# Kernel tuning notes

Measured on AMD Instinct MI355X. Metric: run time of the kernel, lower is better.

## Reference

```python
import jax, jax.numpy as jnp
import numpy as np

N, M, A, O, F = 4, 64, 64, 5, 256


def _sph_harm_l2(R):
    # real spherical harmonics up to l=2 (9 components) of the unit direction
    r = jnp.linalg.norm(R, axis=-1, keepdims=True)
    u = R / (r + 1e-12)
    x, y, z = u[..., 0], u[..., 1], u[..., 2]
    c1 = 0.4886025119029199
    c2 = 1.0925484305920792
    return jnp.stack([
        jnp.full_like(x, 0.28209479177387814),
        c1 * y, c1 * z, c1 * x,
        c2 * x * y, c2 * y * z,
        0.31539156525252005 * (3.0 * z * z - 1.0),
        c2 * x * z,
        0.5462742152960396 * (x * x - y * y),
    ], axis=-1)  # [..., 9]


def setup_inputs() -> dict:
    key = jax.random.key(0)
    ks = jax.random.split(key, 6)
    return {
        "ao_embeddings": jax.random.normal(ks[0], (N, M, A, O, F), jnp.float32),
        "C": jax.random.normal(ks[1], (N, M, A, O), jnp.float32),
        "S": jax.random.normal(ks[2], (N, A, 3, A, 3), jnp.float32),
        "R": jax.random.normal(ks[3], (N, M, A, 3), jnp.float32),
        "w_stack": jax.random.normal(ks[4], (5, 3, 3), jnp.float32) * 0.5,
        "cgc": jax.random.normal(ks[5], (9, 9, 9), jnp.float32) * 0.1,
    }


def reference(ao_embeddings, C, S, R, w_stack, cgc):
    # mo_features: [n, m, a, o=5, f]
    mo = C[..., None] * ao_embeddings
    # 5-step bilinear transform of the overlap-like tensor S [n, a, 3, b, 3]
    Sc = S
    for i in range(5):
        w = w_stack[i]  # [3, 3]
        Sc = jnp.einsum('ab,cd,kibjd->kiajc', w, w, Sc)
        Sc = jax.nn.swish(Sc)
    filt = jnp.array([[1., 1., 0.], [1., 1., 0.], [0., 0., 1.]], Sc.dtype)
    Sc = filt[None, None, :, None, :] * Sc
    idx = jnp.array([0, 1, 2, 2, 2])  # tf.repeat(repeats=[1, 1, 3]) -> size 5
    Sc = jnp.take(jnp.take(Sc, idx, axis=2), idx, axis=4)  # [n, a, 5, b, 5]
    # message passing over atom pairs: [n, m, b, p=5, f]
    mo = jnp.einsum('nmaof,naobp->nmbpf', mo, Sc)
    # unsorted_segment_sum with segment_ids [0,0,1,2,3] into 9 slots == matmul with one-hot map
    seg = jnp.zeros((5, 9), mo.dtype).at[jnp.arange(5), jnp.array([0, 0, 1, 2, 3])].set(1.0)
    mo = jnp.einsum('nmbpf,pq->nmbqf', mo, seg)  # [n, m, a, 9, f]
    # coupling: sph harmonics * ||C|| (tf.repeat over f == broadcast, folded into einsum)
    Cn = jnp.linalg.norm(C, axis=-1)            # [n, m, a]
    coup = _sph_harm_l2(R) * Cn[..., None]      # [n, m, a, 9]
    # CG contraction + sum over atoms a: [n, m, i=9, f]
    out = jnp.einsum('nmapf,nmak,kip->nmif', mo, coup, cgc)
    return jnp.transpose(out, (0, 1, 3, 2))     # [n, m, f, 9]
```

## Files before the change

kernel.cpp:

```cpp
#include <hip/hip_runtime.h>
#include <math.h>


typedef float v4f __attribute__((ext_vector_type(4)));
static __device__ inline v4f splat4(float s) { return (v4f){s, s, s, s}; }

__global__ void k_sc(const float* __restrict__ S, const float* __restrict__ wst,
                     float* __restrict__ G) {
    int t = blockIdx.x * 128 + threadIdx.x;
    int n = t >> 12;
    int a = (t >> 6) & 63;
    int b = t & 63;
    float M[3][3];
#pragma unroll
    for (int x = 0; x < 3; ++x)
#pragma unroll
        for (int y = 0; y < 3; ++y)
            M[x][y] = S[(((n * 64 + a) * 3 + x) * 64 + b) * 3 + y];
#pragma unroll
    for (int it = 0; it < 5; ++it) {
        float w[3][3];
#pragma unroll
        for (int x = 0; x < 3; ++x)
#pragma unroll
            for (int y = 0; y < 3; ++y)
                w[x][y] = wst[it * 9 + x * 3 + y];
        float T[3][3];
#pragma unroll
        for (int x = 0; x < 3; ++x)
#pragma unroll
            for (int d = 0; d < 3; ++d)
                T[x][d] = w[x][0] * M[0][d] + w[x][1] * M[1][d] + w[x][2] * M[2][d];
#pragma unroll
        for (int x = 0; x < 3; ++x)
#pragma unroll
            for (int c = 0; c < 3; ++c) {
                float v = T[x][0] * w[c][0] + T[x][1] * w[c][1] + T[x][2] * w[c][2];
                M[x][c] = v / (1.f + expf(-v));
            }
    }
    float g0 = M[0][0] + M[0][1];
    float g1 = M[1][0] + M[1][1];
    float gz = M[2][2];
    size_t base = (size_t)n * 12288 + (size_t)b * 64 + a;
    G[base]          = g0;
    G[base + 4096]   = g1;
    G[base + 8192]   = gz;
}

__global__ __launch_bounds__(576) void k_w3(
        const float* __restrict__ C, const float* __restrict__ R,
        const float* __restrict__ cgc, const float* __restrict__ G,
        float* __restrict__ wsW3) {
    __shared__ float s_coup[64 * 9];
    __shared__ float s_D[2 * 9 * 64];
    __shared__ float s_W3[64 * 27];

    const int nm = blockIdx.x;
    const int n = nm >> 6;
    const int tid = threadIdx.x;

    if (tid < 64) {
        const int b = tid;
        const float* rp = R + ((size_t)nm * 64 + b) * 3;
        float x = rp[0], y = rp[1], z = rp[2];
        float rn = sqrtf(x * x + y * y + z * z) + 1e-12f;
        x /= rn; y /= rn; z /= rn;
        const float* cp = C + ((size_t)nm * 64 + b) * 5;
        float cn = 0.f;
#pragma unroll
        for (int o = 0; o < 5; ++o) cn += cp[o] * cp[o];
        cn = sqrtf(cn);
        const float c1 = 0.4886025119029199f;
        const float c2 = 1.0925484305920792f;
        float Y[9];
        Y[0] = 0.28209479177387814f;
        Y[1] = c1 * y;
        Y[2] = c1 * z;
        Y[3] = c1 * x;
        Y[4] = c2 * x * y;
        Y[5] = c2 * y * z;
        Y[6] = 0.31539156525252005f * (3.f * z * z - 1.f);
        Y[7] = c2 * x * z;
        Y[8] = 0.5462742152960396f * (x * x - y * y);
#pragma unroll
        for (int k = 0; k < 9; ++k) s_coup[b * 9 + k] = Y[k] * cn;
    }
    __syncthreads();

    {
        const int b = tid & 63, i = tid >> 6;
        float d0 = 0.f, dz = 0.f;
#pragma unroll
        for (int k = 0; k < 9; ++k) {
            float cp = s_coup[b * 9 + k];
            const float* cg = cgc + k * 81 + i * 9;
            d0 = fmaf(cp, cg[0], d0);
            dz = fmaf(cp, cg[1] + cg[2] + cg[3], dz);
        }
        s_D[(0 * 9 + i) * 64 + b] = d0;
        s_D[(1 * 9 + i) * 64 + b] = dz;
    }
    __syncthreads();

    const int pp = __builtin_amdgcn_readfirstlane(tid >> 6);
    const int lane = tid & 63;
    {
        const int u = pp / 3;
        const int i0 = (pp % 3) * 3;
        const int pm = (u == 2) ? 1 : 0;
        const float* gp = G + (size_t)n * 12288 + (size_t)u * 4096 + lane;
        const float* dp = &s_D[(pm * 9 + i0) * 64];
        float a0 = 0.f, a1 = 0.f, a2 = 0.f;
#pragma unroll 8
        for (int b = 0; b < 64; ++b) {
            float g = gp[b * 64];
            a0 = fmaf(g, dp[b], a0);
            a1 = fmaf(g, dp[64 + b], a1);
            a2 = fmaf(g, dp[128 + b], a2);
        }
        s_W3[lane * 27 + u * 9 + i0 + 0] = a0;
        s_W3[lane * 27 + u * 9 + i0 + 1] = a1;
        s_W3[lane * 27 + u * 9 + i0 + 2] = a2;
    }
    __syncthreads();

    float* wp = wsW3 + (size_t)nm * 1792;
    for (int e = tid; e < 1792; e += 576) {
        int a = e / 28, q = e - a * 28;
        wp[e] = (q < 27) ? s_W3[a * 27 + q] : 0.f;
    }
}

__global__ __launch_bounds__(512) void k_out(
        const float* __restrict__ ao, const float* __restrict__ C,
        const float* __restrict__ wsW3, float* __restrict__ out) {
    __shared__ float s_W3[64 * 28];
    __shared__ float s_C[320];
    const int nm = blockIdx.x;
    const int tid = threadIdx.x;
    {
        const float* wp = wsW3 + (size_t)nm * 1792;
        for (int e = tid; e < 1792; e += 512) s_W3[e] = wp[e];
        const float* cp = C + (size_t)nm * 320;
        for (int e = tid; e < 320; e += 512) s_C[e] = cp[e];
    }
    __syncthreads();

    const int w = tid >> 6;
    const int lane = tid & 63;
    const int fgrp = lane & 7;
    const int agrp = lane >> 3;
    const int f0 = w * 32 + fgrp * 4;
    const float* ap = ao + (size_t)nm * 81920 + (size_t)agrp * 1280 + f0;

    v4f acc[9];
#pragma unroll
    for (int i = 0; i < 9; ++i) acc[i] = splat4(0.f);

#pragma unroll
    for (int t = 0; t < 8; ++t) {
        const int a = agrp + 8 * t;
        const float* aop = ap + t * 10240;
        v4f v0 = *(const v4f*)(aop + 0 * 256);
        v4f v1 = *(const v4f*)(aop + 1 * 256);
        v4f v2 = *(const v4f*)(aop + 2 * 256);
        v4f v3 = *(const v4f*)(aop + 3 * 256);
        v4f v4 = *(const v4f*)(aop + 4 * 256);
        const float* cc = &s_C[a * 5];
        v4f e0 = splat4(cc[0]) * v0;
        v4f e1 = splat4(cc[1]) * v1;
        v4f e2 = splat4(cc[2]) * v2 + splat4(cc[3]) * v3 + splat4(cc[4]) * v4;
        const float* w3 = &s_W3[a * 28];
#pragma unroll
        for (int i = 0; i < 9; ++i)
            acc[i] += splat4(w3[i]) * e0 + splat4(w3[9 + i]) * e1 + splat4(w3[18 + i]) * e2;
    }

#pragma unroll
    for (int mask = 8; mask <= 32; mask <<= 1) {
#pragma unroll
        for (int i = 0; i < 9; ++i) {
#pragma unroll
            for (int j = 0; j < 4; ++j)
                acc[i][j] += __shfl_xor(acc[i][j], mask, 64);
        }
    }

    if (agrp == 0) {
        v4f buf4[9];
        float* bp = (float*)buf4;
#pragma unroll
        for (int j = 0; j < 4; ++j)
#pragma unroll
            for (int i = 0; i < 9; ++i)
                bp[j * 9 + i] = acc[i][j];
        float* op = out + (size_t)nm * 2304 + (size_t)f0 * 9;
#pragma unroll
        for (int q = 0; q < 9; ++q)
            *(v4f*)(op + q * 4) = buf4[q];
    }
}

extern "C" void kernel_launch(void* const* d_in, const int* in_sizes, int n_in,
                              void* d_out, int out_size, void* d_ws, size_t ws_size,
                              hipStream_t stream) {
    (void)in_sizes; (void)n_in; (void)out_size; (void)ws_size;
    const float* ao  = (const float*)d_in[0];
    const float* C   = (const float*)d_in[1];
    const float* S   = (const float*)d_in[2];
    const float* R   = (const float*)d_in[3];
    const float* wst = (const float*)d_in[4];
    const float* cgc = (const float*)d_in[5];
    float* out = (float*)d_out;
    float* ws = (float*)d_ws;
    float* G    = ws;
    float* wsW3 = ws + 49152;

    hipLaunchKernelGGL(k_sc,  dim3(128), dim3(128), 0, stream, S, wst, G);
    hipLaunchKernelGGL(k_w3,  dim3(256), dim3(576), 0, stream, C, R, cgc, G, wsW3);
    hipLaunchKernelGGL(k_out, dim3(256), dim3(512), 0, stream, ao, C, wsW3, out);
}
```

Baseline: 31.57 us.

## Fuse three kernels into one cooperative kernel with grid sync

Merges the S-transform, W3 construction, and output contraction into one cooperative launch of 256 blocks, with a grid-wide sync after the G computation. W3 now stays in shared memory instead of going through a global workspace round trip. This removes two kernel launches and the inter-kernel gaps. In exchange it pays for a grid barrier, only 64 of 512 threads do the S stage, and the W3 stage shrinks from 576 to 512 threads, which adds a second loop pass.

```diff
diff --git a/kernel.cpp b/kernel.cpp
--- a/kernel.cpp
+++ b/kernel.cpp
@@ -1,65 +1,74 @@
 #include <hip/hip_runtime.h>
+#include <hip/hip_cooperative_groups.h>
 #include <math.h>
+
+namespace cg = cooperative_groups;
 
 
 typedef float v4f __attribute__((ext_vector_type(4)));
 static __device__ inline v4f splat4(float s) { return (v4f){s, s, s, s}; }
 
-__global__ void k_sc(const float* __restrict__ S, const float* __restrict__ wst,
-                     float* __restrict__ G) {
-    int t = blockIdx.x * 128 + threadIdx.x;
-    int n = t >> 12;
-    int a = (t >> 6) & 63;
-    int b = t & 63;
-    float M[3][3];
-#pragma unroll
-    for (int x = 0; x < 3; ++x)
-#pragma unroll
-        for (int y = 0; y < 3; ++y)
-            M[x][y] = S[(((n * 64 + a) * 3 + x) * 64 + b) * 3 + y];
-#pragma unroll
-    for (int it = 0; it < 5; ++it) {
-        float w[3][3];
-#pragma unroll
-        for (int x = 0; x < 3; ++x)
-#pragma unroll
-            for (int y = 0; y < 3; ++y)
-                w[x][y] = wst[it * 9 + x * 3 + y];
-        float T[3][3];
-#pragma unroll
-        for (int x = 0; x < 3; ++x)
-#pragma unroll
-            for (int d = 0; d < 3; ++d)
-                T[x][d] = w[x][0] * M[0][d] + w[x][1] * M[1][d] + w[x][2] * M[2][d];
-#pragma unroll
-        for (int x = 0; x < 3; ++x)
-#pragma unroll
-            for (int c = 0; c < 3; ++c) {
-                float v = T[x][0] * w[c][0] + T[x][1] * w[c][1] + T[x][2] * w[c][2];
-                M[x][c] = v / (1.f + expf(-v));
-            }
-    }
-    float g0 = M[0][0] + M[0][1];
-    float g1 = M[1][0] + M[1][1];
-    float gz = M[2][2];
-    size_t base = (size_t)n * 12288 + (size_t)b * 64 + a;
-    G[base]          = g0;
-    G[base + 4096]   = g1;
-    G[base + 8192]   = gz;
-}
-
-__global__ __launch_bounds__(576) void k_w3(
-        const float* __restrict__ C, const float* __restrict__ R,
-        const float* __restrict__ cgc, const float* __restrict__ G,
-        float* __restrict__ wsW3) {
+__global__ __launch_bounds__(512) void k_fused(
+        const float* __restrict__ ao, const float* __restrict__ C,
+        const float* __restrict__ S, const float* __restrict__ R,
+        const float* __restrict__ wst, const float* __restrict__ cgc,
+        float* __restrict__ G, float* __restrict__ out) {
     __shared__ float s_coup[64 * 9];
     __shared__ float s_D[2 * 9 * 64];
-    __shared__ float s_W3[64 * 27];
-
-    const int nm = blockIdx.x;
+    __shared__ float s_W3[64 * 28];
+    __shared__ float s_C[320];
+
+    const int blk = blockIdx.x;
+    const int tid = threadIdx.x;
+
+    if (tid < 64) {
+        const int t = blk * 64 + tid;
+        const int n = t >> 12;
+        const int a = (t >> 6) & 63;
+        const int b = t & 63;
+        float M[3][3];
+#pragma unroll
+        for (int x = 0; x < 3; ++x)
+#pragma unroll
+            for (int y = 0; y < 3; ++y)
+                M[x][y] = S[(((n * 64 + a) * 3 + x) * 64 + b) * 3 + y];
+#pragma unroll
+        for (int it = 0; it < 5; ++it) {
+            float w[3][3];
+#pragma unroll
+            for (int x = 0; x < 3; ++x)
+#pragma unroll
+                for (int y = 0; y < 3; ++y)
+                    w[x][y] = wst[it * 9 + x * 3 + y];
+            float T[3][3];
+#pragma unroll
+            for (int x = 0; x < 3; ++x)
+#pragma unroll
+                for (int d = 0; d < 3; ++d)
+                    T[x][d] = w[x][0] * M[0][d] + w[x][1] * M[1][d] + w[x][2] * M[2][d];
+#pragma unroll
+            for (int x = 0; x < 3; ++x)
+#pragma unroll
+                for (int c = 0; c < 3; ++c) {
+                    float v = T[x][0] * w[c][0] + T[x][1] * w[c][1] + T[x][2] * w[c][2];
+                    M[x][c] = v / (1.f + expf(-v));
+                }
+        }
+        const float g0 = M[0][0] + M[0][1];
+        const float g1 = M[1][0] + M[1][1];
+        const float gz = M[2][2];
+        const size_t base = (size_t)n * 12288 + (size_t)b * 64 + a;
+        G[base]        = g0;
+        G[base + 4096] = g1;
+        G[base + 8192] = gz;
+    }
+    __threadfence();
+    cg::this_grid().sync();
+
+    const int nm = blk;
     const int n = nm >> 6;
-    const int tid = threadIdx.x;
-
+
+    for (int e = tid; e < 320; e += 512) s_C[e] = C[(size_t)nm * 320 + e];
     if (tid < 64) {
         const int b = tid;
         const float* rp = R + ((size_t)nm * 64 + b) * 3;
@@ -88,8 +97,8 @@
     }
     __syncthreads();
 
-    {
-        const int b = tid & 63, i = tid >> 6;
+    for (int e = tid; e < 576; e += 512) {
+        const int b = e & 63, i = e >> 6;
         float d0 = 0.f, dz = 0.f;
 #pragma unroll
         for (int k = 0; k < 9; ++k) {
@@ -103,9 +112,9 @@
     }
     __syncthreads();
 
-    const int pp = __builtin_amdgcn_readfirstlane(tid >> 6);
+    const int wid = __builtin_amdgcn_readfirstlane(tid >> 6);
     const int lane = tid & 63;
-    {
+    for (int pp = wid; pp < 9; pp += 8) {
         const int u = pp / 3;
         const int i0 = (pp % 3) * 3;
         const int pm = (u == 2) ? 1 : 0;
@@ -119,36 +128,13 @@
             a1 = fmaf(g, dp[64 + b], a1);
             a2 = fmaf(g, dp[128 + b], a2);
         }
-        s_W3[lane * 27 + u * 9 + i0 + 0] = a0;
-        s_W3[lane * 27 + u * 9 + i0 + 1] = a1;
-        s_W3[lane * 27 + u * 9 + i0 + 2] = a2;
+        s_W3[lane * 28 + u * 9 + i0 + 0] = a0;
+        s_W3[lane * 28 + u * 9 + i0 + 1] = a1;
+        s_W3[lane * 28 + u * 9 + i0 + 2] = a2;
     }
     __syncthreads();
 
-    float* wp = wsW3 + (size_t)nm * 1792;
-    for (int e = tid; e < 1792; e += 576) {
-        int a = e / 28, q = e - a * 28;
-        wp[e] = (q < 27) ? s_W3[a * 27 + q] : 0.f;
-    }
-}
-
-__global__ __launch_bounds__(512) void k_out(
-        const float* __restrict__ ao, const float* __restrict__ C,
-        const float* __restrict__ wsW3, float* __restrict__ out) {
-    __shared__ float s_W3[64 * 28];
-    __shared__ float s_C[320];
-    const int nm = blockIdx.x;
-    const int tid = threadIdx.x;
-    {
-        const float* wp = wsW3 + (size_t)nm * 1792;
-        for (int e = tid; e < 1792; e += 512) s_W3[e] = wp[e];
-        const float* cp = C + (size_t)nm * 320;
-        for (int e = tid; e < 320; e += 512) s_C[e] = cp[e];
-    }
-    __syncthreads();
-
     const int w = tid >> 6;
-    const int lane = tid & 63;
     const int fgrp = lane & 7;
     const int agrp = lane >> 3;
     const int f0 = w * 32 + fgrp * 4;
@@ -213,11 +199,10 @@
     const float* wst = (const float*)d_in[4];
     const float* cgc = (const float*)d_in[5];
     float* out = (float*)d_out;
-    float* ws = (float*)d_ws;
-    float* G    = ws;
-    float* wsW3 = ws + 49152;
-
-    hipLaunchKernelGGL(k_sc,  dim3(128), dim3(128), 0, stream, S, wst, G);
-    hipLaunchKernelGGL(k_w3,  dim3(256), dim3(576), 0, stream, C, R, cgc, G, wsW3);
-    hipLaunchKernelGGL(k_out, dim3(256), dim3(512), 0, stream, ao, C, wsW3, out);
+    float* G = (float*)d_ws;
+
+    void* args[] = {(void*)&ao, (void*)&C, (void*)&S, (void*)&R,
+                    (void*)&wst, (void*)&cgc, (void*)&G, (void*)&out};
+    hipLaunchCooperativeKernel((void*)k_fused, dim3(256), dim3(512),
+                               args, 0, stream);
 }
```

New measurement: 101.9 us. 223% more time.

## Fuse W3 computation into output kernel with split-f blocks and prefetched ao loads

Applied to the files above, without the earlier changes.

Merges the k_w3 and k_out kernels into one k_go kernel, so the per-(n,m) W3 table stays in shared memory instead of going through a workspace round trip, and one launch is removed. The grid doubles to 512 blocks by splitting the feature dimension in halves. Each block issues its first ao loads before the W3 setup phase and software-pipelines the remaining loads across iterations. The cost is that each f-half block recomputes W3 redundantly, and registers grow with the prefetch buffers.

```diff
diff --git a/kernel.cpp b/kernel.cpp
--- a/kernel.cpp
+++ b/kernel.cpp
@@ -48,18 +48,33 @@
     G[base + 8192]   = gz;
 }
 
-__global__ __launch_bounds__(576) void k_w3(
-        const float* __restrict__ C, const float* __restrict__ R,
-        const float* __restrict__ cgc, const float* __restrict__ G,
-        float* __restrict__ wsW3) {
+__global__ __launch_bounds__(512, 4) void k_go(
+        const float* __restrict__ ao, const float* __restrict__ C,
+        const float* __restrict__ R, const float* __restrict__ cgc,
+        const float* __restrict__ G, float* __restrict__ out) {
     __shared__ float s_coup[64 * 9];
     __shared__ float s_D[2 * 9 * 64];
-    __shared__ float s_W3[64 * 27];
-
-    const int nm = blockIdx.x;
+    __shared__ float s_W3[64 * 28];
+    __shared__ float s_C[320];
+
+    const int bid = blockIdx.x;
+    const int nm = bid >> 1;
+    const int fh = bid & 1;
     const int n = nm >> 6;
     const int tid = threadIdx.x;
-
+    const int w = tid >> 6;
+    const int lane = tid & 63;
+    const int fgrp = lane & 3;
+    const int agrp = lane >> 2;
+    const int f0 = fh * 128 + w * 16 + fgrp * 4;
+    const float* ap = ao + (size_t)nm * 81920 + (size_t)agrp * 1280 + f0;
+
+    v4f cur[5];
+#pragma unroll
+    for (int o = 0; o < 5; ++o)
+        cur[o] = *(const v4f*)(ap + o * 256);
+
+    for (int e = tid; e < 320; e += 512) s_C[e] = C[(size_t)nm * 320 + e];
     if (tid < 64) {
         const int b = tid;
         const float* rp = R + ((size_t)nm * 64 + b) * 3;
@@ -88,8 +103,8 @@
     }
     __syncthreads();
 
-    {
-        const int b = tid & 63, i = tid >> 6;
+    for (int e = tid; e < 576; e += 512) {
+        const int b = e & 63, i = e >> 6;
         float d0 = 0.f, dz = 0.f;
 #pragma unroll
         for (int k = 0; k < 9; ++k) {
@@ -103,9 +118,7 @@
     }
     __syncthreads();
 
-    const int pp = __builtin_amdgcn_readfirstlane(tid >> 6);
-    const int lane = tid & 63;
-    {
+    for (int pp = w; pp < 9; pp += 8) {
         const int u = pp / 3;
         const int i0 = (pp % 3) * 3;
         const int pm = (u == 2) ? 1 : 0;
@@ -119,66 +132,42 @@
             a1 = fmaf(g, dp[64 + b], a1);
             a2 = fmaf(g, dp[128 + b], a2);
         }
-        s_W3[lane * 27 + u * 9 + i0 + 0] = a0;
-        s_W3[lane * 27 + u * 9 + i0 + 1] = a1;
-        s_W3[lane * 27 + u * 9 + i0 + 2] = a2;
+        s_W3[lane * 28 + u * 9 + i0 + 0] = a0;
+        s_W3[lane * 28 + u * 9 + i0 + 1] = a1;
+        s_W3[lane * 28 + u * 9 + i0 + 2] = a2;
     }
     __syncthreads();
 
-    float* wp = wsW3 + (size_t)nm * 1792;
-    for (int e = tid; e < 1792; e += 576) {
-        int a = e / 28, q = e - a * 28;
-        wp[e] = (q < 27) ? s_W3[a * 27 + q] : 0.f;
-    }
-}
-
-__global__ __launch_bounds__(512) void k_out(
-        const float* __restrict__ ao, const float* __restrict__ C,
-        const float* __restrict__ wsW3, float* __restrict__ out) {
-    __shared__ float s_W3[64 * 28];
-    __shared__ float s_C[320];
-    const int nm = blockIdx.x;
-    const int tid = threadIdx.x;
-    {
-        const float* wp = wsW3 + (size_t)nm * 1792;
-        for (int e = tid; e < 1792; e += 512) s_W3[e] = wp[e];
-        const float* cp = C + (size_t)nm * 320;
-        for (int e = tid; e < 320; e += 512) s_C[e] = cp[e];
-    }
-    __syncthreads();
-
-    const int w = tid >> 6;
-    const int lane = tid & 63;
-    const int fgrp = lane & 7;
-    const int agrp = lane >> 3;
-    const int f0 = w * 32 + fgrp * 4;
-    const float* ap = ao + (size_t)nm * 81920 + (size_t)agrp * 1280 + f0;
-
     v4f acc[9];
 #pragma unroll
     for (int i = 0; i < 9; ++i) acc[i] = splat4(0.f);
 
 #pragma unroll
-    for (int t = 0; t < 8; ++t) {
-        const int a = agrp + 8 * t;
-        const float* aop = ap + t * 10240;
-        v4f v0 = *(const v4f*)(aop + 0 * 256);
-        v4f v1 = *(const v4f*)(aop + 1 * 256);
-        v4f v2 = *(const v4f*)(aop + 2 * 256);
-        v4f v3 = *(const v4f*)(aop + 3 * 256);
-        v4f v4 = *(const v4f*)(aop + 4 * 256);
+    for (int t = 0; t < 4; ++t) {
+        v4f nxt[5];
+        if (t < 3) {
+            const float* apn = ap + (t + 1) * 20480;
+#pragma unroll
+            for (int o = 0; o < 5; ++o)
+                nxt[o] = *(const v4f*)(apn + o * 256);
+        }
+        const int a = agrp + 16 * t;
         const float* cc = &s_C[a * 5];
-        v4f e0 = splat4(cc[0]) * v0;
-        v4f e1 = splat4(cc[1]) * v1;
-        v4f e2 = splat4(cc[2]) * v2 + splat4(cc[3]) * v3 + splat4(cc[4]) * v4;
+        v4f e0 = splat4(cc[0]) * cur[0];
+        v4f e1 = splat4(cc[1]) * cur[1];
+        v4f e2 = splat4(cc[2]) * cur[2] + splat4(cc[3]) * cur[3] + splat4(cc[4]) * cur[4];
         const float* w3 = &s_W3[a * 28];
 #pragma unroll
         for (int i = 0; i < 9; ++i)
             acc[i] += splat4(w3[i]) * e0 + splat4(w3[9 + i]) * e1 + splat4(w3[18 + i]) * e2;
-    }
-
-#pragma unroll
-    for (int mask = 8; mask <= 32; mask <<= 1) {
+        if (t < 3) {
+#pragma unroll
+            for (int o = 0; o < 5; ++o) cur[o] = nxt[o];
+        }
+    }
+
+#pragma unroll
+    for (int mask = 4; mask <= 32; mask <<= 1) {
 #pragma unroll
         for (int i = 0; i < 9; ++i) {
 #pragma unroll
@@ -213,11 +202,9 @@
     const float* wst = (const float*)d_in[4];
     const float* cgc = (const float*)d_in[5];
     float* out = (float*)d_out;
-    float* ws = (float*)d_ws;
-    float* G    = ws;
-    float* wsW3 = ws + 49152;
-
-    hipLaunchKernelGGL(k_sc,  dim3(128), dim3(128), 0, stream, S, wst, G);
-    hipLaunchKernelGGL(k_w3,  dim3(256), dim3(576), 0, stream, C, R, cgc, G, wsW3);
-    hipLaunchKernelGGL(k_out, dim3(256), dim3(512), 0, stream, ao, C, wsW3, out);
+    float* G = (float*)d_ws;
+
+    hipLaunchKernelGGL(k_sc, dim3(128), dim3(128), 0, stream, S, wst, G);
+    hipLaunchKernelGGL(k_go, dim3(512), dim3(512), 0, stream,
+                       ao, C, R, cgc, G, out);
 }
```

New measurement: 31.52 us. About the same (-0.2%).
